# Optimization experiments

Measured on AMD Instinct MI355X. Metric: run time of the kernel, lower is better.

The kernel has to match this reference:

```python
import jax, jax.numpy as jnp
import numpy as np

PADDING = 1

def setup_inputs() -> dict:
    key = jax.random.key(0)
    k1, k2 = jax.random.split(key)
    imgs = jax.random.normal(k1, (8, 32, 32, 32), dtype=jnp.float32)
    kernel = jax.random.normal(k2, (32, 32, 3, 3), dtype=jnp.float32)
    return {"imgs": imgs, "kernel": kernel}

def reference(imgs, kernel):
    # Tropical max-plus 'convolution' (kind='conv': kernel spatially flipped),
    # groups=1, stride=1, dilation=1, padding=PADDING with semifield zero = -inf.
    B, C, H, W = imgs.shape
    O, Ck, kh, kw = kernel.shape
    OY = H + 2 * PADDING - (kh - 1)
    OX = W + 2 * PADDING - (kw - 1)
    neg_inf = jnp.array(-jnp.inf, dtype=imgs.dtype)
    x = jnp.pad(imgs, ((0, 0), (0, 0), (PADDING, PADDING), (PADDING, PADDING)),
                constant_values=neg_inf)
    # conv flips the kernel spatially
    k = kernel[:, :, ::-1, ::-1]
    # im2col windows: [B, C, kh*kw, OY, OX] (small fixed loop over kernel taps)
    windows = jnp.stack(
        [x[:, :, dy:dy + OY, dx:dx + OX] for dy in range(kh) for dx in range(kw)],
        axis=2,
    )
    # broadcast 'multiply' (tropical: add): [B, O, C, kh*kw, OY, OX]
    mult = windows[:, None] + k.reshape(1, O, C, kh * kw, 1, 1)
    # tropical add-reduce (max) over channels and kernel taps
    out = jnp.max(mult, axis=(2, 3))  # [B, O, OY, OX]
    return out
```

## Files before the change

### kernel.cpp

```cpp
#include <hip/hip_runtime.h>
#include <math.h>


constexpr int B = 8, C = 32, O = 32, H = 32, W = 32;

__device__ __forceinline__ float f3(float a, float b, float c) {
  return fmaxf(fmaxf(a, b), c);
}

__global__ __launch_bounds__(256, 4) void trop_conv_kernel(
    const float* __restrict__ img, const float* __restrict__ kern,
    float* __restrict__ out) {
  __shared__ float sw[32 * 16];

  const int tid = threadIdx.x;
  const int blk = blockIdx.x;
  const int yq = blk & 3;
  const int o = (blk >> 2) & 31;
  const int b = blk >> 7;

  const float* kw = kern + o * 288;
  for (int j = tid; j < 288; j += 256) {
    int c = j / 9;
    int t = j - c * 9;
    sw[c * 16 + t] = kw[j];
  }
  __syncthreads();

  const int x = tid & 31;
  const int r = tid >> 5;
  const int y = yq * 8 + r;

  int ro0, ro1, ro2;
  {
    int ym = y - 1; ym = ym < 0 ? 0 : ym;
    int yp = y + 1; yp = yp > 31 ? 31 : yp;
    ro0 = ym * W + x;
    ro1 = y * W + x;
    ro2 = yp * W + x;
  }
  const bool top_oob = (y == 0);
  const bool bot_oob = (y == 31);
  const bool xz = (x == 0);
  const bool xe = (x == 31);
  const float NEG = -__builtin_huge_valf();

  const float* ib = img + b * C * H * W;

  float acc = NEG;

#pragma unroll 8
  for (int c = 0; c < C; ++c) {
    const float* ic = ib + c * H * W;
    float v0 = ic[ro0];
    float v1 = ic[ro1];
    float v2 = ic[ro2];
    v0 = top_oob ? NEG : v0;
    v2 = bot_oob ? NEG : v2;

    float l0 = __shfl_up(v0, 1), r0 = __shfl_down(v0, 1);
    float l1 = __shfl_up(v1, 1), r1 = __shfl_down(v1, 1);
    float l2 = __shfl_up(v2, 1), r2 = __shfl_down(v2, 1);
    l0 = xz ? NEG : l0;  r0 = xe ? NEG : r0;
    l1 = xz ? NEG : l1;  r1 = xe ? NEG : r1;
    l2 = xz ? NEG : l2;  r2 = xe ? NEG : r2;

    const float4 A0 = *(const float4*)&sw[c * 16];
    const float4 A1 = *(const float4*)&sw[c * 16 + 4];
    const float A8 = sw[c * 16 + 8];

    float t0 = f3(l0 + A8,   v0 + A1.w, r0 + A1.z);
    float t1 = f3(l1 + A1.y, v1 + A1.x, r1 + A0.w);
    float t2 = f3(l2 + A0.z, v2 + A0.y, r2 + A0.x);
    acc = fmaxf(acc, f3(t0, t1, t2));
  }

  out[((b * O + o) * H + y) * W + x] = acc;
}

extern "C" void kernel_launch(void* const* d_in, const int* in_sizes, int n_in,
                              void* d_out, int out_size, void* d_ws, size_t ws_size,
                              hipStream_t stream) {
  const float* img = (const float*)d_in[0];
  const float* kern = (const float*)d_in[1];
  float* out = (float*)d_out;
  trop_conv_kernel<<<dim3(1024), dim3(256), 0, stream>>>(img, kern, out);
}
```

Baseline: 69.05 us.

## Compute two outputs per thread with vector row loads, drop shared-memory weights

Each thread now computes two adjacent output pixels from three 4-wide unaligned vector loads per channel, replacing the wave shuffles with register selects for halo handling. Kernel weights are read straight from global (uniform, likely scalar loads) instead of being staged in LDS, which removes the syncthreads. The grid is halved to 512 blocks, each covering 16 rows. The cost is fewer waves in flight and more select instructions per channel.

```diff
diff --git a/kernel.cpp b/kernel.cpp
--- a/kernel.cpp
+++ b/kernel.cpp
@@ -3,79 +3,99 @@
 
 
 constexpr int B = 8, C = 32, O = 32, H = 32, W = 32;
+constexpr int HW = H * W;
+
+typedef float f4 __attribute__((ext_vector_type(4)));
 
 __device__ __forceinline__ float f3(float a, float b, float c) {
   return fmaxf(fmaxf(a, b), c);
 }
 
-__global__ __launch_bounds__(256, 4) void trop_conv_kernel(
+__device__ __forceinline__ f4 ld4u(const float* p) {
+  f4 q;
+  __builtin_memcpy(&q, p, sizeof(q));
+  return q;
+}
+
+__global__ __launch_bounds__(256, 2) void trop_conv_kernel(
     const float* __restrict__ img, const float* __restrict__ kern,
     float* __restrict__ out) {
-  __shared__ float sw[32 * 16];
-
   const int tid = threadIdx.x;
   const int blk = blockIdx.x;
-  const int yq = blk & 3;
-  const int o = (blk >> 2) & 31;
-  const int b = blk >> 7;
+  const int yh = blk & 1;
+  const int o = (blk >> 1) & 31;
+  const int b = blk >> 6;
 
-  const float* kw = kern + o * 288;
-  for (int j = tid; j < 288; j += 256) {
-    int c = j / 9;
-    int t = j - c * 9;
-    sw[c * 16 + t] = kw[j];
-  }
-  __syncthreads();
+  const int seg = tid & 15;
+  const int x0 = seg * 2;
+  const int r = tid >> 4;
+  const int y = yh * 16 + r;
 
-  const int x = tid & 31;
-  const int r = tid >> 5;
-  const int y = yq * 8 + r;
+  int xb = x0 - 1;
+  xb = xb < 0 ? 0 : xb;
+  xb = xb > 28 ? 28 : xb;
+  int ym = y - 1; ym = ym < 0 ? 0 : ym;
+  int yp = y + 1; yp = yp > 31 ? 31 : yp;
+  const int off0 = ym * W + xb;
+  const int off1 = y * W + xb;
+  const int off2 = yp * W + xb;
 
-  int ro0, ro1, ro2;
-  {
-    int ym = y - 1; ym = ym < 0 ? 0 : ym;
-    int yp = y + 1; yp = yp > 31 ? 31 : yp;
-    ro0 = ym * W + x;
-    ro1 = y * W + x;
-    ro2 = yp * W + x;
-  }
-  const bool top_oob = (y == 0);
-  const bool bot_oob = (y == 31);
-  const bool xz = (x == 0);
-  const bool xe = (x == 31);
+  const bool top = (y == 0);
+  const bool bot = (y == 31);
+  const bool xz = (x0 == 0);
+  const bool xe = (x0 == 30);
   const float NEG = -__builtin_huge_valf();
 
-  const float* ib = img + b * C * H * W;
+  const float* ib = img + b * C * HW;
+  const float* kc = kern + o * 288;
 
-  float acc = NEG;
+  float acc0 = NEG, acc1 = NEG;
 
-#pragma unroll 8
+#pragma unroll 4
   for (int c = 0; c < C; ++c) {
-    const float* ic = ib + c * H * W;
-    float v0 = ic[ro0];
-    float v1 = ic[ro1];
-    float v2 = ic[ro2];
-    v0 = top_oob ? NEG : v0;
-    v2 = bot_oob ? NEG : v2;
+    const float* ic = ib + c * HW;
+    const float* kp = kc + c * 9;
+    const float w0 = kp[0], w1 = kp[1], w2 = kp[2], w3 = kp[3], w4 = kp[4],
+                w5 = kp[5], w6 = kp[6], w7 = kp[7], w8 = kp[8];
 
-    float l0 = __shfl_up(v0, 1), r0 = __shfl_down(v0, 1);
-    float l1 = __shfl_up(v1, 1), r1 = __shfl_down(v1, 1);
-    float l2 = __shfl_up(v2, 1), r2 = __shfl_down(v2, 1);
-    l0 = xz ? NEG : l0;  r0 = xe ? NEG : r0;
-    l1 = xz ? NEG : l1;  r1 = xe ? NEG : r1;
-    l2 = xz ? NEG : l2;  r2 = xe ? NEG : r2;
+    const f4 q0 = ld4u(ic + off0);
+    const f4 q1 = ld4u(ic + off1);
+    const f4 q2 = ld4u(ic + off2);
 
-    const float4 A0 = *(const float4*)&sw[c * 16];
-    const float4 A1 = *(const float4*)&sw[c * 16 + 4];
-    const float A8 = sw[c * 16 + 8];
+    const float am = xz ? NEG : (xe ? q0.y : q0.x);
+    const float a0 = xe ? q0.z : (xz ? q0.x : q0.y);
+    const float a1 = xe ? q0.w : (xz ? q0.y : q0.z);
+    const float a2 = xe ? NEG : (xz ? q0.z : q0.w);
 
-    float t0 = f3(l0 + A8,   v0 + A1.w, r0 + A1.z);
-    float t1 = f3(l1 + A1.y, v1 + A1.x, r1 + A0.w);
-    float t2 = f3(l2 + A0.z, v2 + A0.y, r2 + A0.x);
-    acc = fmaxf(acc, f3(t0, t1, t2));
+    const float bm = xz ? NEG : (xe ? q1.y : q1.x);
+    const float b0 = xe ? q1.z : (xz ? q1.x : q1.y);
+    const float b1 = xe ? q1.w : (xz ? q1.y : q1.z);
+    const float b2 = xe ? NEG : (xz ? q1.z : q1.w);
+
+    const float cm = xz ? NEG : (xe ? q2.y : q2.x);
+    const float c0 = xe ? q2.z : (xz ? q2.x : q2.y);
+    const float c1 = xe ? q2.w : (xz ? q2.y : q2.z);
+    const float c2 = xe ? NEG : (xz ? q2.z : q2.w);
+
+    float t0a = f3(am + w8, a0 + w7, a1 + w6);
+    float t1a = f3(a0 + w8, a1 + w7, a2 + w6);
+    t0a = top ? NEG : t0a;
+    t1a = top ? NEG : t1a;
+
+    const float t0b = f3(bm + w5, b0 + w4, b1 + w3);
+    const float t1b = f3(b0 + w5, b1 + w4, b2 + w3);
+
+    float t0c = f3(cm + w2, c0 + w1, c1 + w0);
+    float t1c = f3(c0 + w2, c1 + w1, c2 + w0);
+    t0c = bot ? NEG : t0c;
+    t1c = bot ? NEG : t1c;
+
+    acc0 = fmaxf(acc0, f3(t0a, t0b, t0c));
+    acc1 = fmaxf(acc1, f3(t1a, t1b, t1c));
   }
 
-  out[((b * O + o) * H + y) * W + x] = acc;
+  float2 res = make_float2(acc0, acc1);
+  *reinterpret_cast<float2*>(&out[((b * O + o) * H + y) * W + x0]) = res;
 }
 
 extern "C" void kernel_launch(void* const* d_in, const int* in_sizes, int n_in,
@@ -84,5 +104,5 @@
   const float* img = (const float*)d_in[0];
   const float* kern = (const float*)d_in[1];
   float* out = (float*)d_out;
-  trop_conv_kernel<<<dim3(1024), dim3(256), 0, stream>>>(img, kern, out);
+  trop_conv_kernel<<<dim3(512), dim3(256), 0, stream>>>(img, kern, out);
 }
```

After: 63.58 us. 7.9% less time.
